# Performance work log

Measured on AMD Instinct MI355X. Metric: run time of the kernel, lower is better.

The kernel has to match this reference:

```python
import jax, jax.numpy as jnp
import numpy as np

# Block-sparse layout constants (must match init_kwargs):
BS = 64       # block_size (= block_m = block_n)
NB = 64       # number of blocks per side -> max_seqlen = 4096
LOCAL = 8     # causal sliding window of 8 blocks
GLOBAL = 1    # 1 global (attention-sink) block


def _layout():
    """Build padded per-row block column indices and the token-level mask.

    Mirrors dkernel semantics: block (i, j) participates iff sparse_pattern[i, j] == 1,
    and within participating blocks a per-token causal mask (k_pos <= q_pos) is applied
    (dkernel applies causal masking on diagonal blocks; off-diagonal lower blocks pass
    the causal test trivially, so pattern & causal is exact).
    """
    i = np.arange(NB)[:, None]
    j = np.arange(NB)[None, :]
    pat = (j <= i) & (((i - j) < LOCAL) | (j < GLOBAL))  # [NB, NB] bool
    max_nnz = int(pat.sum(-1).max())                      # = LOCAL + GLOBAL = 9
    col = np.zeros((NB, max_nnz), np.int32)
    valid = np.zeros((NB, max_nnz), bool)
    for r in range(NB):
        idx = np.nonzero(pat[r])[0]
        col[r, :len(idx)] = idx
        valid[r, :len(idx)] = True
    # token positions
    qpos = np.arange(NB)[:, None] * BS + np.arange(BS)[None, :]                    # [NB, BS]
    kpos = (col[:, :, None] * BS + np.arange(BS)[None, None, :]).reshape(NB, -1)   # [NB, max_nnz*BS]
    vmask = np.repeat(valid, BS, axis=1)                                           # [NB, max_nnz*BS]
    mask = vmask[:, None, :] & (kpos[:, None, :] <= qpos[:, :, None])              # [NB, BS, max_nnz*BS]
    return col, mask

_COL, _MASK = _layout()


def setup_inputs() -> dict:
    key = jax.random.key(0)
    kq, kk, kv = jax.random.split(key, 3)
    B, S, H, D = 2, 4096, 16, 128
    q = jax.random.normal(kq, (B, S, H, D), dtype=jnp.float32)
    k = jax.random.normal(kk, (B, S, H, D), dtype=jnp.float32)
    v = jax.random.normal(kv, (B, S, H, D), dtype=jnp.float32)
    return {"q": q, "k": k, "v": v}


def reference(q, k, v):
    B, S, H, D = q.shape
    sm_scale = 1.0 / np.sqrt(float(D))  # default sm_scale in forward()
    # -> [B, H, NB, BS, D]
    qb = q.reshape(B, NB, BS, H, D).transpose(0, 3, 1, 2, 4)
    kb = k.reshape(B, NB, BS, H, D).transpose(0, 3, 1, 2, 4)
    vb = v.reshape(B, NB, BS, H, D).transpose(0, 3, 1, 2, 4)
    col = jnp.asarray(_COL)                              # [NB, max_nnz]
    # gather the kv blocks each q-block attends to: [B, H, NB, max_nnz*BS, D]
    kg = kb[:, :, col].reshape(B, H, NB, -1, D)
    vg = vb[:, :, col].reshape(B, H, NB, -1, D)
    # block-sparse scores: [B, H, NB, BS, max_nnz*BS]
    s = jnp.einsum('bhnqd,bhnkd->bhnqk', qb, kg) * sm_scale
    s = jnp.where(jnp.asarray(_MASK)[None, None], s, -jnp.inf)
    p = jax.nn.softmax(s, axis=-1)
    o = jnp.einsum('bhnqk,bhnkd->bhnqd', p, vg)          # [B, H, NB, BS, D]
    return o.transpose(0, 2, 3, 1, 4).reshape(B, S, H, D)
```

## Files before the change

kernel.cpp:

```cpp
#include <hip/hip_runtime.h>
#include <hip/hip_bf16.h>


typedef __bf16 bf16_t;
typedef bf16_t bf16x8 __attribute__((ext_vector_type(8)));
typedef bf16_t bf16x4 __attribute__((ext_vector_type(4)));
typedef float f32x4 __attribute__((ext_vector_type(4)));
typedef uint32_t u32x4 __attribute__((ext_vector_type(4)));

#define BSZ 64
#define DIM 128
#define NH 16
#define SEQ 4096
#define ROWSTRIDE (NH * DIM)

#define LGKM_BARRIER()                                          \
    do {                                                        \
        asm volatile("s_waitcnt lgkmcnt(0)" ::: "memory");      \
        __builtin_amdgcn_s_barrier();                           \
        __builtin_amdgcn_sched_barrier(0);                      \
    } while (0)

__device__ __forceinline__ uint32_t kb_swz(uint32_t A) {
    return A ^ (((A >> 8) & 7u) << 4);
}
__device__ __forceinline__ uint32_t vt_swz(uint32_t A) {
    return A ^ (((A >> 9) & 7u) << 4) ^ (((A >> 8) & 1u) << 6);
}

__global__ __launch_bounds__(256) void sparse_attn_kernel(
    const float* __restrict__ q, const float* __restrict__ k,
    const float* __restrict__ v, float* __restrict__ out)
{
    __shared__ __align__(16) bf16_t Kb[BSZ * DIM];
    __shared__ __align__(16) bf16_t Vt[DIM * BSZ];

    const int L  = ((blockIdx.x & 7) << 8) | (blockIdx.x >> 3);
    const int qi = L & 63;
    const int h  = (L >> 6) & 15;
    const int b  = L >> 10;

    const int tid  = threadIdx.x;
    const int wave = tid >> 6;
    const int lane = tid & 63;
    const int lr = lane & 15;
    const int lk = lane >> 4;
    const int k0 = lk * 8;

    const int sc4 = tid & 31;
    const int sr  = tid >> 5;

    const float scale2 = 0.12751649736230476f;

    const size_t bh_off = ((size_t)b * SEQ * NH + (size_t)h) * DIM;
    const float* kbh = k + bh_off;
    const float* vbh = v + bh_off;

    bf16x8 qf[4];
    {
        const float* qrow = q + bh_off + (size_t)(qi * 64 + wave * 16 + lr) * ROWSTRIDE;
        #pragma unroll
        for (int kk = 0; kk < 4; ++kk) {
            const float4 a0 = *(const float4*)(qrow + 32 * kk + k0);
            const float4 a1 = *(const float4*)(qrow + 32 * kk + k0 + 4);
            bf16x8 f;
            f[0] = (bf16_t)(a0.x * scale2); f[1] = (bf16_t)(a0.y * scale2);
            f[2] = (bf16_t)(a0.z * scale2); f[3] = (bf16_t)(a0.w * scale2);
            f[4] = (bf16_t)(a1.x * scale2); f[5] = (bf16_t)(a1.y * scale2);
            f[6] = (bf16_t)(a1.z * scale2); f[7] = (bf16_t)(a1.w * scale2);
            qf[kk] = f;
        }
    }

    f32x4 oacc[8];
    #pragma unroll
    for (int n = 0; n < 8; ++n) oacc[n] = (f32x4){0.f, 0.f, 0.f, 0.f};
    float mrun = -3.0e38f, lrun = 0.f;

    const int qrow_local = wave * 16 + lr;
    const int nnz = (qi < 8) ? (qi + 1) : 9;

    float4 kreg[8];
    float4 vreg[8];

    #define LOAD_K(jb)                                                            \
    {                                                                             \
        const float* kb_ = kbh + (size_t)((jb) * 64) * ROWSTRIDE + 4 * sc4;       \
        _Pragma("unroll")                                                         \
        for (int i = 0; i < 8; ++i)                                               \
            kreg[i] = *(const float4*)(kb_ + (size_t)(8 * i + sr) * ROWSTRIDE);   \
    }
    #define LOAD_V(jb)                                                            \
    {                                                                             \
        const float* vb_ = vbh + (size_t)((jb) * 64) * ROWSTRIDE + 4 * sc4;       \
        _Pragma("unroll")                                                         \
        for (int T = 0; T < 2; ++T)                                               \
            _Pragma("unroll")                                                     \
            for (int i = 0; i < 4; ++i)                                           \
                vreg[T * 4 + i] = *(const float4*)(vb_ +                          \
                    (size_t)(4 * (sr + 8 * T) + i) * ROWSTRIDE);                  \
    }

    LOAD_K(0);

    for (int t = 0; t < nnz; ++t) {
        const int j = (qi < 8) ? t : ((t == 0) ? 0 : (qi - 8 + t));

        LOAD_V(j);

        #pragma unroll
        for (int i = 0; i < 8; ++i) {
            const float4 t4 = kreg[i];
            bf16x4 c = {(bf16_t)t4.x, (bf16_t)t4.y, (bf16_t)t4.z, (bf16_t)t4.w};
            const uint32_t A = kb_swz((uint32_t)((8 * i + sr) * 256 + 8 * sc4));
            *(bf16x4*)((char*)Kb + A) = c;
        }
        LGKM_BARRIER();

        f32x4 sacc[4];
        __builtin_amdgcn_s_setprio(1);
        #pragma unroll
        for (int n = 0; n < 4; ++n) {
            f32x4 a = (f32x4){0.f, 0.f, 0.f, 0.f};
            #pragma unroll
            for (int kk = 0; kk < 4; ++kk) {
                const uint32_t A = kb_swz((uint32_t)((16 * n + lr) * 256 + 64 * kk + 16 * lk));
                bf16x8 kf = *(const bf16x8*)((const char*)Kb + A);
                a = __builtin_amdgcn_mfma_f32_16x16x32_bf16(kf, qf[kk], a, 0, 0, 0);
            }
            sacc[n] = a;
        }
        __builtin_amdgcn_s_setprio(0);

        #pragma unroll
        for (int T = 0; T < 2; ++T) {
            #pragma unroll
            for (int j2 = 0; j2 < 4; ++j2) {
                const int d = 4 * sc4 + j2;
                bf16x4 c = {(bf16_t)((const float*)&vreg[T * 4 + 0])[j2],
                            (bf16_t)((const float*)&vreg[T * 4 + 1])[j2],
                            (bf16_t)((const float*)&vreg[T * 4 + 2])[j2],
                            (bf16_t)((const float*)&vreg[T * 4 + 3])[j2]};
                const uint32_t A = vt_swz((uint32_t)(d * 128 + 8 * (sr + 8 * T)));
                *(bf16x4*)((char*)Vt + A) = c;
            }
        }

        if (j == qi) {
            #pragma unroll
            for (int n = 0; n < 4; ++n)
                #pragma unroll
                for (int r = 0; r < 4; ++r) {
                    if (16 * n + 4 * lk + r > qrow_local) sacc[n][r] = -1.0e30f;
                }
        }
        float vmax = -3.0e38f;
        #pragma unroll
        for (int n = 0; n < 4; ++n)
            #pragma unroll
            for (int r = 0; r < 4; ++r) vmax = fmaxf(vmax, sacc[n][r]);
        vmax = fmaxf(vmax, __shfl_xor(vmax, 16));
        vmax = fmaxf(vmax, __shfl_xor(vmax, 32));

        if (!__all(vmax - mrun <= 8.0f)) {
            const float mnew = fmaxf(mrun, vmax);
            const float alpha = exp2f(mrun - mnew);
            mrun = mnew;
            lrun *= alpha;
            float av[4];
            #pragma unroll
            for (int r = 0; r < 4; ++r) av[r] = __shfl(alpha, 4 * lk + r);
            #pragma unroll
            for (int n = 0; n < 8; ++n)
                #pragma unroll
                for (int r = 0; r < 4; ++r) oacc[n][r] *= av[r];
        }
        uint32_t ch[8];
        #pragma unroll
        for (int n = 0; n < 4; ++n) {
            float p0 = exp2f(sacc[n][0] - mrun);
            float p1 = exp2f(sacc[n][1] - mrun);
            float p2 = exp2f(sacc[n][2] - mrun);
            float p3 = exp2f(sacc[n][3] - mrun);
            lrun += (p0 + p1) + (p2 + p3);
            bf16x4 c4 = {(bf16_t)p0, (bf16_t)p1, (bf16_t)p2, (bf16_t)p3};
            uint32_t* cw = (uint32_t*)&c4;
            ch[2 * n]     = cw[0];
            ch[2 * n + 1] = cw[1];
        }

        bf16x8 paf[2];
        {
            const int s0 = lr + 32 * (lk & 1);
            const bool hi = (lk & 2) != 0;
            #pragma unroll
            for (int kk = 0; kk < 2; ++kk) {
                uint32_t res[4];
                #pragma unroll
                for (int u = 0; u < 2; ++u) {
                    const uint32_t a0 = (uint32_t)__shfl((int)ch[4 * kk + u],     s0);
                    const uint32_t b0 = (uint32_t)__shfl((int)ch[4 * kk + 2 + u], s0);
                    const uint32_t a1 = (uint32_t)__shfl((int)ch[4 * kk + u],     s0 + 16);
                    const uint32_t b1 = (uint32_t)__shfl((int)ch[4 * kk + 2 + u], s0 + 16);
                    res[u]     = hi ? b0 : a0;
                    res[2 + u] = hi ? b1 : a1;
                }
                u32x4 tv = {res[0], res[1], res[2], res[3]};
                paf[kk] = *(bf16x8*)&tv;
            }
        }

        if (t + 1 < nnz) {
            const int jn = (qi < 8) ? (t + 1) : (qi - 8 + t + 1);
            LOAD_K(jn);
        }
        LGKM_BARRIER();

        __builtin_amdgcn_s_setprio(1);
        #pragma unroll
        for (int n = 0; n < 8; ++n) {
            f32x4 a = oacc[n];
            #pragma unroll
            for (int kk = 0; kk < 2; ++kk) {
                const uint32_t Av = vt_swz((uint32_t)((16 * n + lr) * 128 + 64 * kk + 16 * lk));
                bf16x8 vf = *(const bf16x8*)((const char*)Vt + Av);
                a = __builtin_amdgcn_mfma_f32_16x16x32_bf16(paf[kk], vf, a, 0, 0, 0);
            }
            oacc[n] = a;
        }
        __builtin_amdgcn_s_setprio(0);
    }

    float lrtot = lrun;
    lrtot += __shfl_xor(lrtot, 16);
    lrtot += __shfl_xor(lrtot, 32);
    float* obase = out + bh_off + (size_t)(qi * 64 + wave * 16) * ROWSTRIDE;
    #pragma unroll
    for (int r = 0; r < 4; ++r) {
        const float inv = 1.0f / __shfl(lrtot, 4 * lk + r);
        float* orow = obase + (size_t)(4 * lk + r) * ROWSTRIDE;
        #pragma unroll
        for (int n = 0; n < 8; ++n) {
            orow[16 * n + lr] = oacc[n][r] * inv;
        }
    }
}

extern "C" void kernel_launch(void* const* d_in, const int* in_sizes, int n_in,
                              void* d_out, int out_size, void* d_ws, size_t ws_size,
                              hipStream_t stream) {
    const float* q = (const float*)d_in[0];
    const float* k = (const float*)d_in[1];
    const float* v = (const float*)d_in[2];
    float* out = (float*)d_out;
    sparse_attn_kernel<<<dim3(2048), dim3(256), 0, stream>>>(q, k, v, out);
}
```

Baseline: 105.6 us.

## Process two adjacent query blocks per workgroup to share K/V block loads

Each workgroup now handles two consecutive 64-row query blocks, with each wave owning 32 query rows from one of them. The union of the two blocks' KV windows (10 blocks instead of 2×9) is streamed once through shared memory, and each wave skips the blocks outside its own window. This cuts global K/V traffic and fp32-to-bf16 conversion work roughly in half and halves the grid size. The cost is doubled per-wave accumulator and register state, which may lower occupancy, and idle waves on non-shared iterations.

```diff
diff --git a/kernel.cpp b/kernel.cpp
--- a/kernel.cpp
+++ b/kernel.cpp
@@ -35,10 +35,10 @@
     __shared__ __align__(16) bf16_t Kb[BSZ * DIM];
     __shared__ __align__(16) bf16_t Vt[DIM * BSZ];
 
-    const int L  = ((blockIdx.x & 7) << 8) | (blockIdx.x >> 3);
-    const int qi = L & 63;
-    const int h  = (L >> 6) & 15;
-    const int b  = L >> 10;
+    const int L  = ((blockIdx.x & 7) << 7) | (blockIdx.x >> 3);
+    const int g  = L & 31;
+    const int h  = (L >> 5) & 15;
+    const int b  = L >> 9;
 
     const int tid  = threadIdx.x;
     const int wave = tid >> 6;
@@ -47,6 +47,9 @@
     const int lk = lane >> 4;
     const int k0 = lk * 8;
 
+    const int myblk = 2 * g + (wave >> 1);
+    const int qbase = (wave & 1) * 32;
+
     const int sc4 = tid & 31;
     const int sr  = tid >> 5;
 
@@ -56,9 +59,11 @@
     const float* kbh = k + bh_off;
     const float* vbh = v + bh_off;
 
-    bf16x8 qf[4];
-    {
-        const float* qrow = q + bh_off + (size_t)(qi * 64 + wave * 16 + lr) * ROWSTRIDE;
+    bf16x8 qf[2][4];
+    #pragma unroll
+    for (int m = 0; m < 2; ++m) {
+        const float* qrow = q + bh_off +
+            (size_t)(myblk * 64 + qbase + 16 * m + lr) * ROWSTRIDE;
         #pragma unroll
         for (int kk = 0; kk < 4; ++kk) {
             const float4 a0 = *(const float4*)(qrow + 32 * kk + k0);
@@ -68,17 +73,19 @@
             f[2] = (bf16_t)(a0.z * scale2); f[3] = (bf16_t)(a0.w * scale2);
             f[4] = (bf16_t)(a1.x * scale2); f[5] = (bf16_t)(a1.y * scale2);
             f[6] = (bf16_t)(a1.z * scale2); f[7] = (bf16_t)(a1.w * scale2);
-            qf[kk] = f;
-        }
-    }
-
-    f32x4 oacc[8];
+            qf[m][kk] = f;
+        }
+    }
+
+    f32x4 oacc[2][8];
     #pragma unroll
-    for (int n = 0; n < 8; ++n) oacc[n] = (f32x4){0.f, 0.f, 0.f, 0.f};
-    float mrun = -3.0e38f, lrun = 0.f;
-
-    const int qrow_local = wave * 16 + lr;
-    const int nnz = (qi < 8) ? (qi + 1) : 9;
+    for (int m = 0; m < 2; ++m)
+        #pragma unroll
+        for (int n = 0; n < 8; ++n) oacc[m][n] = (f32x4){0.f, 0.f, 0.f, 0.f};
+    float mrun[2] = {-3.0e38f, -3.0e38f}, lrun[2] = {0.f, 0.f};
+
+    const int lo  = (2 * g - 7 > 1) ? (2 * g - 7) : 1;
+    const int nit = 2 * g + 3 - lo;
 
     float4 kreg[8];
     float4 vreg[8];
@@ -103,8 +110,9 @@
 
     LOAD_K(0);
 
-    for (int t = 0; t < nnz; ++t) {
-        const int j = (qi < 8) ? t : ((t == 0) ? 0 : (qi - 8 + t));
+    for (int t = 0; t < nit; ++t) {
+        const int j = (t == 0) ? 0 : (lo + t - 1);
+        const bool act = (j == 0) || (j >= myblk - 7 && j <= myblk);
 
         LOAD_V(j);
 
@@ -117,20 +125,25 @@
         }
         LGKM_BARRIER();
 
-        f32x4 sacc[4];
-        __builtin_amdgcn_s_setprio(1);
-        #pragma unroll
-        for (int n = 0; n < 4; ++n) {
-            f32x4 a = (f32x4){0.f, 0.f, 0.f, 0.f};
-            #pragma unroll
-            for (int kk = 0; kk < 4; ++kk) {
-                const uint32_t A = kb_swz((uint32_t)((16 * n + lr) * 256 + 64 * kk + 16 * lk));
-                bf16x8 kf = *(const bf16x8*)((const char*)Kb + A);
-                a = __builtin_amdgcn_mfma_f32_16x16x32_bf16(kf, qf[kk], a, 0, 0, 0);
-            }
-            sacc[n] = a;
-        }
-        __builtin_amdgcn_s_setprio(0);
+        f32x4 sacc[2][4];
+        if (act) {
+            __builtin_amdgcn_s_setprio(1);
+            #pragma unroll
+            for (int n = 0; n < 4; ++n) {
+                f32x4 a0 = (f32x4){0.f, 0.f, 0.f, 0.f};
+                f32x4 a1 = (f32x4){0.f, 0.f, 0.f, 0.f};
+                #pragma unroll
+                for (int kk = 0; kk < 4; ++kk) {
+                    const uint32_t A = kb_swz((uint32_t)((16 * n + lr) * 256 + 64 * kk + 16 * lk));
+                    bf16x8 kf = *(const bf16x8*)((const char*)Kb + A);
+                    a0 = __builtin_amdgcn_mfma_f32_16x16x32_bf16(kf, qf[0][kk], a0, 0, 0, 0);
+                    a1 = __builtin_amdgcn_mfma_f32_16x16x32_bf16(kf, qf[1][kk], a1, 0, 0, 0);
+                }
+                sacc[0][n] = a0;
+                sacc[1][n] = a1;
+            }
+            __builtin_amdgcn_s_setprio(0);
+        }
 
         #pragma unroll
         for (int T = 0; T < 2; ++T) {
@@ -146,102 +159,118 @@
             }
         }
 
-        if (j == qi) {
-            #pragma unroll
-            for (int n = 0; n < 4; ++n)
-                #pragma unroll
-                for (int r = 0; r < 4; ++r) {
-                    if (16 * n + 4 * lk + r > qrow_local) sacc[n][r] = -1.0e30f;
-                }
-        }
-        float vmax = -3.0e38f;
-        #pragma unroll
-        for (int n = 0; n < 4; ++n)
-            #pragma unroll
-            for (int r = 0; r < 4; ++r) vmax = fmaxf(vmax, sacc[n][r]);
-        vmax = fmaxf(vmax, __shfl_xor(vmax, 16));
-        vmax = fmaxf(vmax, __shfl_xor(vmax, 32));
-
-        if (!__all(vmax - mrun <= 8.0f)) {
-            const float mnew = fmaxf(mrun, vmax);
-            const float alpha = exp2f(mrun - mnew);
-            mrun = mnew;
-            lrun *= alpha;
-            float av[4];
-            #pragma unroll
-            for (int r = 0; r < 4; ++r) av[r] = __shfl(alpha, 4 * lk + r);
-            #pragma unroll
-            for (int n = 0; n < 8; ++n)
-                #pragma unroll
-                for (int r = 0; r < 4; ++r) oacc[n][r] *= av[r];
-        }
-        uint32_t ch[8];
-        #pragma unroll
-        for (int n = 0; n < 4; ++n) {
-            float p0 = exp2f(sacc[n][0] - mrun);
-            float p1 = exp2f(sacc[n][1] - mrun);
-            float p2 = exp2f(sacc[n][2] - mrun);
-            float p3 = exp2f(sacc[n][3] - mrun);
-            lrun += (p0 + p1) + (p2 + p3);
-            bf16x4 c4 = {(bf16_t)p0, (bf16_t)p1, (bf16_t)p2, (bf16_t)p3};
-            uint32_t* cw = (uint32_t*)&c4;
-            ch[2 * n]     = cw[0];
-            ch[2 * n + 1] = cw[1];
-        }
-
-        bf16x8 paf[2];
-        {
-            const int s0 = lr + 32 * (lk & 1);
-            const bool hi = (lk & 2) != 0;
-            #pragma unroll
-            for (int kk = 0; kk < 2; ++kk) {
-                uint32_t res[4];
-                #pragma unroll
-                for (int u = 0; u < 2; ++u) {
-                    const uint32_t a0 = (uint32_t)__shfl((int)ch[4 * kk + u],     s0);
-                    const uint32_t b0 = (uint32_t)__shfl((int)ch[4 * kk + 2 + u], s0);
-                    const uint32_t a1 = (uint32_t)__shfl((int)ch[4 * kk + u],     s0 + 16);
-                    const uint32_t b1 = (uint32_t)__shfl((int)ch[4 * kk + 2 + u], s0 + 16);
-                    res[u]     = hi ? b0 : a0;
-                    res[2 + u] = hi ? b1 : a1;
-                }
-                u32x4 tv = {res[0], res[1], res[2], res[3]};
-                paf[kk] = *(bf16x8*)&tv;
-            }
-        }
-
-        if (t + 1 < nnz) {
-            const int jn = (qi < 8) ? (t + 1) : (qi - 8 + t + 1);
-            LOAD_K(jn);
-        }
+        bf16x8 paf[2][2];
+        if (act) {
+            const bool diag = (j == myblk);
+            float vmax[2];
+            #pragma unroll
+            for (int m = 0; m < 2; ++m) {
+                if (diag) {
+                    const int qrl = qbase + 16 * m + lr;
+                    #pragma unroll
+                    for (int n = 0; n < 4; ++n)
+                        #pragma unroll
+                        for (int r = 0; r < 4; ++r)
+                            if (16 * n + 4 * lk + r > qrl) sacc[m][n][r] = -1.0e30f;
+                }
+                float vm = -3.0e38f;
+                #pragma unroll
+                for (int n = 0; n < 4; ++n)
+                    #pragma unroll
+                    for (int r = 0; r < 4; ++r) vm = fmaxf(vm, sacc[m][n][r]);
+                vm = fmaxf(vm, __shfl_xor(vm, 16));
+                vm = fmaxf(vm, __shfl_xor(vm, 32));
+                vmax[m] = vm;
+            }
+            if (!__all(vmax[0] - mrun[0] <= 8.0f && vmax[1] - mrun[1] <= 8.0f)) {
+                #pragma unroll
+                for (int m = 0; m < 2; ++m) {
+                    const float mnew = fmaxf(mrun[m], vmax[m]);
+                    const float alpha = exp2f(mrun[m] - mnew);
+                    mrun[m] = mnew;
+                    lrun[m] *= alpha;
+                    float av[4];
+                    #pragma unroll
+                    for (int r = 0; r < 4; ++r) av[r] = __shfl(alpha, 4 * lk + r);
+                    #pragma unroll
+                    for (int n = 0; n < 8; ++n)
+                        #pragma unroll
+                        for (int r = 0; r < 4; ++r) oacc[m][n][r] *= av[r];
+                }
+            }
+            #pragma unroll
+            for (int m = 0; m < 2; ++m) {
+                uint32_t ch[8];
+                #pragma unroll
+                for (int n = 0; n < 4; ++n) {
+                    float p0 = exp2f(sacc[m][n][0] - mrun[m]);
+                    float p1 = exp2f(sacc[m][n][1] - mrun[m]);
+                    float p2 = exp2f(sacc[m][n][2] - mrun[m]);
+                    float p3 = exp2f(sacc[m][n][3] - mrun[m]);
+                    lrun[m] += (p0 + p1) + (p2 + p3);
+                    bf16x4 c4 = {(bf16_t)p0, (bf16_t)p1, (bf16_t)p2, (bf16_t)p3};
+                    uint32_t* cw = (uint32_t*)&c4;
+                    ch[2 * n]     = cw[0];
+                    ch[2 * n + 1] = cw[1];
+                }
+                const int s0 = lr + 32 * (lk & 1);
+                const bool hi = (lk & 2) != 0;
+                #pragma unroll
+                for (int kk = 0; kk < 2; ++kk) {
+                    uint32_t res[4];
+                    #pragma unroll
+                    for (int u = 0; u < 2; ++u) {
+                        const uint32_t a0 = (uint32_t)__shfl((int)ch[4 * kk + u],     s0);
+                        const uint32_t b0 = (uint32_t)__shfl((int)ch[4 * kk + 2 + u], s0);
+                        const uint32_t a1 = (uint32_t)__shfl((int)ch[4 * kk + u],     s0 + 16);
+                        const uint32_t b1 = (uint32_t)__shfl((int)ch[4 * kk + 2 + u], s0 + 16);
+                        res[u]     = hi ? b0 : a0;
+                        res[2 + u] = hi ? b1 : a1;
+                    }
+                    u32x4 tv = {res[0], res[1], res[2], res[3]};
+                    paf[m][kk] = *(bf16x8*)&tv;
+                }
+            }
+        }
+
+        if (t + 1 < nit) { LOAD_K(lo + t); }
         LGKM_BARRIER();
 
-        __builtin_amdgcn_s_setprio(1);
-        #pragma unroll
-        for (int n = 0; n < 8; ++n) {
-            f32x4 a = oacc[n];
-            #pragma unroll
-            for (int kk = 0; kk < 2; ++kk) {
-                const uint32_t Av = vt_swz((uint32_t)((16 * n + lr) * 128 + 64 * kk + 16 * lk));
-                bf16x8 vf = *(const bf16x8*)((const char*)Vt + Av);
-                a = __builtin_amdgcn_mfma_f32_16x16x32_bf16(paf[kk], vf, a, 0, 0, 0);
-            }
-            oacc[n] = a;
-        }
-        __builtin_amdgcn_s_setprio(0);
-    }
-
-    float lrtot = lrun;
-    lrtot += __shfl_xor(lrtot, 16);
-    lrtot += __shfl_xor(lrtot, 32);
-    float* obase = out + bh_off + (size_t)(qi * 64 + wave * 16) * ROWSTRIDE;
+        if (act) {
+            __builtin_amdgcn_s_setprio(1);
+            #pragma unroll
+            for (int n = 0; n < 8; ++n) {
+                f32x4 a0 = oacc[0][n];
+                f32x4 a1 = oacc[1][n];
+                #pragma unroll
+                for (int kk = 0; kk < 2; ++kk) {
+                    const uint32_t Av = vt_swz((uint32_t)((16 * n + lr) * 128 + 64 * kk + 16 * lk));
+                    bf16x8 vf = *(const bf16x8*)((const char*)Vt + Av);
+                    a0 = __builtin_amdgcn_mfma_f32_16x16x32_bf16(paf[0][kk], vf, a0, 0, 0, 0);
+                    a1 = __builtin_amdgcn_mfma_f32_16x16x32_bf16(paf[1][kk], vf, a1, 0, 0, 0);
+                }
+                oacc[0][n] = a0;
+                oacc[1][n] = a1;
+            }
+            __builtin_amdgcn_s_setprio(0);
+        }
+    }
+
     #pragma unroll
-    for (int r = 0; r < 4; ++r) {
-        const float inv = 1.0f / __shfl(lrtot, 4 * lk + r);
-        float* orow = obase + (size_t)(4 * lk + r) * ROWSTRIDE;
-        #pragma unroll
-        for (int n = 0; n < 8; ++n) {
-            orow[16 * n + lr] = oacc[n][r] * inv;
+    for (int m = 0; m < 2; ++m) {
+        float lt = lrun[m];
+        lt += __shfl_xor(lt, 16);
+        lt += __shfl_xor(lt, 32);
+        float* obase = out + bh_off +
+            (size_t)(myblk * 64 + qbase + 16 * m) * ROWSTRIDE;
+        #pragma unroll
+        for (int r = 0; r < 4; ++r) {
+            const float inv = 1.0f / __shfl(lt, 4 * lk + r);
+            float* orow = obase + (size_t)(4 * lk + r) * ROWSTRIDE;
+            #pragma unroll
+            for (int n = 0; n < 8; ++n) {
+                orow[16 * n + lr] = oacc[m][n][r] * inv;
+            }
         }
     }
 }
@@ -253,5 +282,5 @@
     const float* k = (const float*)d_in[1];
     const float* v = (const float*)d_in[2];
     float* out = (float*)d_out;
-    sparse_attn_kernel<<<dim3(2048), dim3(256), 0, stream>>>(q, k, v, out);
-}
+    sparse_attn_kernel<<<dim3(1024), dim3(256), 0, stream>>>(q, k, v, out);
+}
```

Result: slower. 144.5 us (+36.8%).

## Double-buffer K/V shared tiles and prefetch two blocks ahead

Applied to the files above, without the earlier changes.

Doubles the LDS buffers for K and transposed V and restructures the loop so the next block's bf16 conversion and LDS write happen after the PV MMA, while global loads for the block after that are issued. This cuts the per-iteration barriers from two to one and gives the global loads more time in flight. The cost is twice the LDS (64KB per block), which may reduce occupancy, plus extra registers held for prefetched data.

```diff
diff --git a/kernel.cpp b/kernel.cpp
--- a/kernel.cpp
+++ b/kernel.cpp
@@ -32,8 +32,8 @@
     const float* __restrict__ q, const float* __restrict__ k,
     const float* __restrict__ v, float* __restrict__ out)
 {
-    __shared__ __align__(16) bf16_t Kb[BSZ * DIM];
-    __shared__ __align__(16) bf16_t Vt[DIM * BSZ];
+    __shared__ __align__(16) bf16_t Kb[2 * BSZ * DIM];
+    __shared__ __align__(16) bf16_t Vt[2 * DIM * BSZ];
 
     const int L  = ((blockIdx.x & 7) << 8) | (blockIdx.x >> 3);
     const int qi = L & 63;
@@ -100,22 +100,48 @@
                 vreg[T * 4 + i] = *(const float4*)(vb_ +                          \
                     (size_t)(4 * (sr + 8 * T) + i) * ROWSTRIDE);                  \
     }
+    #define KB_WRITE(cc)                                                          \
+    {                                                                             \
+        _Pragma("unroll")                                                         \
+        for (int i = 0; i < 8; ++i) {                                             \
+            const float4 t4 = kreg[i];                                            \
+            bf16x4 cq = {(bf16_t)t4.x, (bf16_t)t4.y, (bf16_t)t4.z, (bf16_t)t4.w};\
+            const uint32_t A = kb_swz((uint32_t)((8 * i + sr) * 256 + 8 * sc4));  \
+            *(bf16x4*)((char*)Kb + (cc) * 16384 + A) = cq;                        \
+        }                                                                         \
+    }
+    #define VT_WRITE(cc)                                                          \
+    {                                                                             \
+        _Pragma("unroll")                                                         \
+        for (int T = 0; T < 2; ++T) {                                             \
+            _Pragma("unroll")                                                     \
+            for (int j2 = 0; j2 < 4; ++j2) {                                      \
+                const int d = 4 * sc4 + j2;                                       \
+                bf16x4 cq = {(bf16_t)((const float*)&vreg[T * 4 + 0])[j2],        \
+                             (bf16_t)((const float*)&vreg[T * 4 + 1])[j2],        \
+                             (bf16_t)((const float*)&vreg[T * 4 + 2])[j2],        \
+                             (bf16_t)((const float*)&vreg[T * 4 + 3])[j2]};       \
+                const uint32_t A = vt_swz((uint32_t)(d * 128 + 8 * (sr + 8 * T)));\
+                *(bf16x4*)((char*)Vt + (cc) * 16384 + A) = cq;                    \
+            }                                                                     \
+        }                                                                         \
+    }
 
     LOAD_K(0);
-
+    LOAD_V(0);
+    KB_WRITE(0);
+    VT_WRITE(0);
+    if (nnz > 1) {
+        const int j1 = (qi < 8) ? 1 : (qi - 7);
+        LOAD_K(j1);
+        LOAD_V(j1);
+    }
+    LGKM_BARRIER();
+
+    int c = 0;
     for (int t = 0; t < nnz; ++t) {
         const int j = (qi < 8) ? t : ((t == 0) ? 0 : (qi - 8 + t));
-
-        LOAD_V(j);
-
-        #pragma unroll
-        for (int i = 0; i < 8; ++i) {
-            const float4 t4 = kreg[i];
-            bf16x4 c = {(bf16_t)t4.x, (bf16_t)t4.y, (bf16_t)t4.z, (bf16_t)t4.w};
-            const uint32_t A = kb_swz((uint32_t)((8 * i + sr) * 256 + 8 * sc4));
-            *(bf16x4*)((char*)Kb + A) = c;
-        }
-        LGKM_BARRIER();
+        const uint32_t cOff = (uint32_t)(c * 16384);
 
         f32x4 sacc[4];
         __builtin_amdgcn_s_setprio(1);
@@ -125,26 +151,12 @@
             #pragma unroll
             for (int kk = 0; kk < 4; ++kk) {
                 const uint32_t A = kb_swz((uint32_t)((16 * n + lr) * 256 + 64 * kk + 16 * lk));
-                bf16x8 kf = *(const bf16x8*)((const char*)Kb + A);
+                bf16x8 kf = *(const bf16x8*)((const char*)Kb + cOff + A);
                 a = __builtin_amdgcn_mfma_f32_16x16x32_bf16(kf, qf[kk], a, 0, 0, 0);
             }
             sacc[n] = a;
         }
         __builtin_amdgcn_s_setprio(0);
-
-        #pragma unroll
-        for (int T = 0; T < 2; ++T) {
-            #pragma unroll
-            for (int j2 = 0; j2 < 4; ++j2) {
-                const int d = 4 * sc4 + j2;
-                bf16x4 c = {(bf16_t)((const float*)&vreg[T * 4 + 0])[j2],
-                            (bf16_t)((const float*)&vreg[T * 4 + 1])[j2],
-                            (bf16_t)((const float*)&vreg[T * 4 + 2])[j2],
-                            (bf16_t)((const float*)&vreg[T * 4 + 3])[j2]};
-                const uint32_t A = vt_swz((uint32_t)(d * 128 + 8 * (sr + 8 * T)));
-                *(bf16x4*)((char*)Vt + A) = c;
-            }
-        }
 
         if (j == qi) {
             #pragma unroll
@@ -210,12 +222,6 @@
             }
         }
 
-        if (t + 1 < nnz) {
-            const int jn = (qi < 8) ? (t + 1) : (qi - 8 + t + 1);
-            LOAD_K(jn);
-        }
-        LGKM_BARRIER();
-
         __builtin_amdgcn_s_setprio(1);
         #pragma unroll
         for (int n = 0; n < 8; ++n) {
@@ -223,12 +229,24 @@
             #pragma unroll
             for (int kk = 0; kk < 2; ++kk) {
                 const uint32_t Av = vt_swz((uint32_t)((16 * n + lr) * 128 + 64 * kk + 16 * lk));
-                bf16x8 vf = *(const bf16x8*)((const char*)Vt + Av);
+                bf16x8 vf = *(const bf16x8*)((const char*)Vt + cOff + Av);
                 a = __builtin_amdgcn_mfma_f32_16x16x32_bf16(paf[kk], vf, a, 0, 0, 0);
             }
             oacc[n] = a;
         }
         __builtin_amdgcn_s_setprio(0);
+
+        if (t + 1 < nnz) {
+            KB_WRITE(c ^ 1);
+            VT_WRITE(c ^ 1);
+            if (t + 2 < nnz) {
+                const int j2n = (qi < 8) ? (t + 2) : (qi - 8 + t + 2);
+                LOAD_K(j2n);
+                LOAD_V(j2n);
+            }
+        }
+        LGKM_BARRIER();
+        c ^= 1;
     }
 
     float lrtot = lrun;
```

Measured after the change: 114.0 us. 1.08x slower.
